# Kernel tuning notes

Measured on AMD Instinct MI355X. Metric: run time of the kernel, lower is better.

The kernel has to match this reference:

```python
import jax, jax.numpy as jnp
import numpy as np

N_NODES = 50000
N_EDGES = 1600000
SLOPE = 0.01  # LeakyReLU default negative slope


def _leaky(x):
    return jnp.where(x >= 0, x, SLOPE * x)


def _gcn(x, W, b, row, col, num_nodes):
    """PyG GCNConv: x' = D^{-1/2}(A+I)D^{-1/2} X W + b (self-loops already in row/col)."""
    x = x @ W  # [N, 64]
    deg = jax.ops.segment_sum(jnp.ones_like(row, dtype=x.dtype), col, num_segments=num_nodes)
    dinv = jnp.where(deg > 0, jax.lax.rsqrt(deg), 0.0)
    norm = dinv[row] * dinv[col]  # [E+N]
    msg = x[row] * norm[:, None]  # gather + scale, [E+N, 64]
    out = jax.ops.segment_sum(msg, col, num_segments=num_nodes)
    return out + b


def setup_inputs() -> dict:
    key = jax.random.key(0)
    ks = jax.random.split(key, 24)
    d = {}
    d["screen"] = jax.random.normal(ks[0], (N_NODES, 768), jnp.float32)
    d["des"] = jax.random.normal(ks[1], (N_NODES, 768), jnp.float32)
    d["tweet"] = jax.random.normal(ks[2], (N_NODES, 768), jnp.float32)
    d["profile"] = jax.random.normal(ks[3], (N_NODES, 5), jnp.float32)
    d["personal"] = jax.random.normal(ks[4], (N_NODES, 7), jnp.float32)
    d["edge"] = jax.random.randint(ks[5], (2, N_EDGES), 0, N_NODES, dtype=jnp.int32)

    def lin(k, fan_in, fan_out):
        s = 1.0 / np.sqrt(fan_in)
        k1, k2 = jax.random.split(k)
        W = jax.random.uniform(k1, (fan_in, fan_out), jnp.float32, -s, s)
        b = jax.random.uniform(k2, (fan_out,), jnp.float32, -s, s)
        return W, b

    d["W_screen"], d["b_screen"] = lin(ks[6], 768, 16)
    d["W_des"], d["b_des"] = lin(ks[7], 768, 16)
    d["W_tweet"], d["b_tweet"] = lin(ks[8], 768, 16)
    d["W_pro"], d["b_pro"] = lin(ks[9], 5, 8)
    d["W_per"], d["b_per"] = lin(ks[10], 7, 8)
    d["W_lin"], d["b_lin"] = lin(ks[11], 64, 64)
    d["W_g1"], d["b_g1"] = lin(ks[12], 64, 64)
    d["W_g2"], d["b_g2"] = lin(ks[13], 64, 64)
    d["W_g3"], d["b_g3"] = lin(ks[14], 64, 64)
    d["W_o1"], d["b_o1"] = lin(ks[15], 64, 64)
    d["W_o2"], d["b_o2"] = lin(ks[16], 64, 2)
    return d


def reference(screen, des, tweet, profile, personal, edge,
              W_screen, b_screen, W_des, b_des, W_tweet, b_tweet,
              W_pro, b_pro, W_per, b_per, W_lin, b_lin,
              W_g1, b_g1, W_g2, b_g2, W_g3, b_g3,
              W_o1, b_o1, W_o2, b_o2):
    n = screen.shape[0]
    # dropout layers act as identity in eval mode
    s = _leaky(screen @ W_screen + b_screen)
    de = _leaky(des @ W_des + b_des)
    t = _leaky(tweet @ W_tweet + b_tweet)
    p = _leaky(profile @ W_pro + b_pro)
    pe = _leaky(personal @ W_per + b_per)
    x1 = jnp.concatenate((s, de, t, p, pe), axis=1)  # [N, 64]
    x = _leaky(x1 @ W_lin + b_lin)
    # add self-loops once (shared by all three GCN layers)
    loops = jnp.arange(n, dtype=edge.dtype)
    row = jnp.concatenate([edge[0], loops])
    col = jnp.concatenate([edge[1], loops])
    x = _gcn(x, W_g1, b_g1, row, col, n) + x1
    x = _gcn(x, W_g2, b_g2, row, col, n) + x1
    x = _gcn(x, W_g3, b_g3, row, col, n) + x1
    x = _leaky(x @ W_o1 + b_o1)
    return jax.nn.sigmoid(x @ W_o2 + b_o2)
```

## Files before the change

### kernel.cpp

```cpp
#include <hip/hip_runtime.h>

__device__ __forceinline__ float leaky(float v) { return v >= 0.f ? v : 0.01f * v; }

__device__ __forceinline__ void fma4(float4& a, float s, const float4& w) {
    a.x = fmaf(s, w.x, a.x); a.y = fmaf(s, w.y, a.y);
    a.z = fmaf(s, w.z, a.z); a.w = fmaf(s, w.w, a.w);
}

__device__ __forceinline__ unsigned short f2bf(float x) {
    unsigned b = __float_as_uint(x);
    return (unsigned short)((b + 0x7FFFu + ((b >> 16) & 1u)) >> 16);
}
__device__ __forceinline__ float bf2f(unsigned short u) {
    return __uint_as_float(((unsigned)u) << 16);
}

typedef __attribute__((ext_vector_type(8))) short short8v;
typedef __attribute__((ext_vector_type(4))) float float4v;

__global__ void k_deg(const int* __restrict__ col, int E, int* __restrict__ deg) {
    int e = blockIdx.x * blockDim.x + threadIdx.x;
    if (e < E) atomicAdd(&deg[col[e]], 1);
}

__global__ __launch_bounds__(256) void k_scan_part(const int* __restrict__ deg,
                                                   int* __restrict__ part,
                                                   int* __restrict__ bsum, int N) {
    __shared__ int tmp[256];
    int tid = threadIdx.x;
    int i = blockIdx.x * 256 + tid;
    int v = (i < N) ? deg[i] : 0;
    tmp[tid] = v;
    __syncthreads();
    for (int ofs = 1; ofs < 256; ofs <<= 1) {
        int t = (tid >= ofs) ? tmp[tid - ofs] : 0;
        __syncthreads();
        tmp[tid] += t;
        __syncthreads();
    }
    int incl = tmp[tid];
    if (i < N) part[i] = incl - v;
    if (tid == 255) bsum[blockIdx.x] = incl;
}

__global__ __launch_bounds__(256) void k_scan_sums(const int* __restrict__ bsum,
                                                   int* __restrict__ boff, int NB,
                                                   int* __restrict__ offs_last) {
    __shared__ int tmp[256];
    int tid = threadIdx.x;
    int v = (tid < NB) ? bsum[tid] : 0;
    tmp[tid] = v;
    __syncthreads();
    for (int ofs = 1; ofs < 256; ofs <<= 1) {
        int t = (tid >= ofs) ? tmp[tid - ofs] : 0;
        __syncthreads();
        tmp[tid] += t;
        __syncthreads();
    }
    int incl = tmp[tid];
    if (tid < NB) boff[tid] = incl - v;
    if (tid == 255) offs_last[0] = incl;
}

__global__ __launch_bounds__(256) void k_scan_final(const int* __restrict__ part,
                                                    const int* __restrict__ boff,
                                                    const int* __restrict__ deg,
                                                    int* __restrict__ offs,
                                                    int* __restrict__ pos,
                                                    float* __restrict__ dinv, int N) {
    int i = blockIdx.x * 256 + threadIdx.x;
    if (i < N) {
        int o = part[i] + boff[blockIdx.x];
        offs[i] = o;
        pos[i] = o;
        dinv[i] = rsqrtf((float)(deg[i] + 1));
    }
}

__global__ void k_fill(const int* __restrict__ row, const int* __restrict__ col, int E,
                       int* __restrict__ pos, int* __restrict__ csr) {
    int e = blockIdx.x * blockDim.x + threadIdx.x;
    if (e < E) {
        int p = atomicAdd(&pos[col[e]], 1);
        csr[p] = row[e];
    }
}

__global__ __launch_bounds__(512) void k_featB(
    const float* __restrict__ s, const float* __restrict__ d, const float* __restrict__ t,
    const float* __restrict__ Ws, const float* __restrict__ bs2,
    const float* __restrict__ Wd, const float* __restrict__ bd2,
    const float* __restrict__ Wt, const float* __restrict__ bt2,
    const float* __restrict__ prof, const float* __restrict__ pers,
    const float* __restrict__ Wp, const float* __restrict__ bp,
    const float* __restrict__ Wpe, const float* __restrict__ bpe,
    float* __restrict__ x1g, int N, int NG) {
    __shared__ short8v wfv[3072];

    const int bid = blockIdx.x;
    const int tid = threadIdx.x;

    if (bid >= 3 * NG) {
        int n = (bid - 3 * NG) * 512 + tid;
        if (n >= N) return;
        float pv[5], pe[7];
#pragma unroll
        for (int i = 0; i < 5; ++i) pv[i] = prof[(size_t)n * 5 + i];
#pragma unroll
        for (int i = 0; i < 7; ++i) pe[i] = pers[(size_t)n * 7 + i];
        float o[16];
#pragma unroll
        for (int j = 0; j < 8; ++j) {
            float a = bp[j];
#pragma unroll
            for (int i = 0; i < 5; ++i) a = fmaf(pv[i], Wp[i * 8 + j], a);
            o[j] = leaky(a);
            float a2 = bpe[j];
#pragma unroll
            for (int i = 0; i < 7; ++i) a2 = fmaf(pe[i], Wpe[i * 8 + j], a2);
            o[8 + j] = leaky(a2);
        }
#pragma unroll
        for (int v = 0; v < 4; ++v)
            *reinterpret_cast<float4*>(x1g + (size_t)n * 64 + 48 + v * 4) =
                make_float4(o[v * 4], o[v * 4 + 1], o[v * 4 + 2], o[v * 4 + 3]);
        return;
    }

    const int f = bid / NG;
    const int grp = bid - f * NG;
    const float* __restrict__ X = (f == 0) ? s : ((f == 1) ? d : t);
    const float* __restrict__ W = (f == 0) ? Ws : ((f == 1) ? Wd : Wt);
    const float* __restrict__ B = (f == 0) ? bs2 : ((f == 1) ? bd2 : bt2);
    const int n0 = grp * 128;
    const int lane = tid & 63;
    const int wid = tid >> 6;

    short* wfs = (short*)wfv;
#pragma unroll
    for (int v = 0; v < 6; ++v) {
        int idx4 = tid + v * 512;
        float4 w4 = *reinterpret_cast<const float4*>(W + (size_t)idx4 * 4);
        int k = idx4 >> 2;
        int j0 = (idx4 & 3) * 4;
        int c = k >> 5, g = (k >> 3) & 3, i = k & 7;
        float wq[4] = {w4.x, w4.y, w4.z, w4.w};
#pragma unroll
        for (int q = 0; q < 4; ++q) {
            int sl = (c * 64 + g * 16 + j0 + q) * 8 + i;
            unsigned short h = f2bf(wq[q]);
            wfs[sl] = (short)h;
            wfs[12288 + sl] = (short)f2bf(wq[q] - bf2f(h));
        }
    }
    __syncthreads();

    const int nb = n0 + wid * 16;
    int mrow = nb + (lane & 15); if (mrow >= N) mrow = N - 1;
    const float* base = X + (size_t)mrow * 768 + ((lane >> 4) << 3);

    float4 pa[4], pb[4];
#pragma unroll
    for (int u = 0; u < 4; ++u) {
        pa[u] = *reinterpret_cast<const float4*>(base + u * 32);
        pb[u] = *reinterpret_cast<const float4*>(base + u * 32 + 4);
    }
    float4v acc = {0.f, 0.f, 0.f, 0.f};

#pragma unroll
    for (int c = 0; c < 24; ++c) {
        const int u = c & 3;
        float xs[8] = {pa[u].x, pa[u].y, pa[u].z, pa[u].w,
                       pb[u].x, pb[u].y, pb[u].z, pb[u].w};
        if (c + 4 < 24) {
            pa[u] = *reinterpret_cast<const float4*>(base + (c + 4) * 32);
            pb[u] = *reinterpret_cast<const float4*>(base + (c + 4) * 32 + 4);
        }
        short8v xh, xl;
#pragma unroll
        for (int i = 0; i < 8; ++i) {
            unsigned short h = f2bf(xs[i]);
            xh[i] = (short)h;
            xl[i] = (short)f2bf(xs[i] - bf2f(h));
        }
        short8v wh = wfv[c * 64 + lane];
        short8v wl = wfv[1536 + c * 64 + lane];
        acc = __builtin_amdgcn_mfma_f32_16x16x32_bf16(xh, wh, acc, 0, 0, 0);
        acc = __builtin_amdgcn_mfma_f32_16x16x32_bf16(xl, wh, acc, 0, 0, 0);
        acc = __builtin_amdgcn_mfma_f32_16x16x32_bf16(xh, wl, acc, 0, 0, 0);
    }

    int j = lane & 15;
    float bb = B[j];
#pragma unroll
    for (int r = 0; r < 4; ++r) {
        int n = nb + ((lane >> 4) << 2) + r;
        if (n < N) x1g[(size_t)n * 64 + f * 16 + j] = leaky(acc[r] + bb);
    }
}

__global__ __launch_bounds__(256) void k_lin1(const float* __restrict__ x1,
                                              const float* __restrict__ Wl,
                                              const float* __restrict__ bl,
                                              const float* __restrict__ Wg1,
                                              const float* __restrict__ dinvv,
                                              unsigned short* __restrict__ z, int N) {
    __shared__ float4 xt4[1024];
    __shared__ float4 wt4[1024];
    const int tid = threadIdx.x;
    const int n0 = blockIdx.x * 64;
    const int nq = tid & 15;
    const int jq = tid >> 4;

#pragma unroll
    for (int v = 0; v < 4; ++v) {
        int L = v * 256 + tid;
        int n = L >> 4, c4 = L & 15;
        int nn = n0 + n; if (nn >= N) nn = N - 1;
        xt4[n * 16 + (c4 ^ (n & 15))] = *reinterpret_cast<const float4*>(x1 + (size_t)nn * 64 + c4 * 4);
        wt4[L] = *reinterpret_cast<const float4*>(Wl + (size_t)L * 4);
    }
    __syncthreads();

    float4 acc[4];
#pragma unroll
    for (int g = 0; g < 4; ++g) acc[g] = make_float4(0.f, 0.f, 0.f, 0.f);
    for (int k = 0; k < 64; k += 4) {
        float4 w0 = wt4[(k + 0) * 16 + jq];
        float4 w1 = wt4[(k + 1) * 16 + jq];
        float4 w2 = wt4[(k + 2) * 16 + jq];
        float4 w3 = wt4[(k + 3) * 16 + jq];
        int k4 = k >> 2;
#pragma unroll
        for (int g = 0; g < 4; ++g) {
            int n = nq + (g << 4);
            float4 xv = xt4[n * 16 + (k4 ^ (n & 15))];
            fma4(acc[g], xv.x, w0);
            fma4(acc[g], xv.y, w1);
            fma4(acc[g], xv.z, w2);
            fma4(acc[g], xv.w, w3);
        }
    }
    float4 bb = *reinterpret_cast<const float4*>(bl + jq * 4);
    __syncthreads();

#pragma unroll
    for (int g = 0; g < 4; ++g) {
        int n = nq + (g << 4);
        float4 h;
        h.x = leaky(acc[g].x + bb.x);
        h.y = leaky(acc[g].y + bb.y);
        h.z = leaky(acc[g].z + bb.z);
        h.w = leaky(acc[g].w + bb.w);
        xt4[n * 16 + (jq ^ (n & 15))] = h;
    }
#pragma unroll
    for (int v = 0; v < 4; ++v) {
        int L = v * 256 + tid;
        wt4[L] = *reinterpret_cast<const float4*>(Wg1 + (size_t)L * 4);
    }
    __syncthreads();

#pragma unroll
    for (int g = 0; g < 4; ++g) acc[g] = make_float4(0.f, 0.f, 0.f, 0.f);
    for (int k = 0; k < 64; k += 4) {
        float4 w0 = wt4[(k + 0) * 16 + jq];
        float4 w1 = wt4[(k + 1) * 16 + jq];
        float4 w2 = wt4[(k + 2) * 16 + jq];
        float4 w3 = wt4[(k + 3) * 16 + jq];
        int k4 = k >> 2;
#pragma unroll
        for (int g = 0; g < 4; ++g) {
            int n = nq + (g << 4);
            float4 xv = xt4[n * 16 + (k4 ^ (n & 15))];
            fma4(acc[g], xv.x, w0);
            fma4(acc[g], xv.y, w1);
            fma4(acc[g], xv.z, w2);
            fma4(acc[g], xv.w, w3);
        }
    }
#pragma unroll
    for (int g = 0; g < 4; ++g) {
        int n = nq + (g << 4);
        if (n0 + n >= N) continue;
        float dv = dinvv[n0 + n];
        ushort4 o;
        o.x = f2bf(acc[g].x * dv); o.y = f2bf(acc[g].y * dv);
        o.z = f2bf(acc[g].z * dv); o.w = f2bf(acc[g].w * dv);
        *reinterpret_cast<ushort4*>(z + (size_t)(n0 + n) * 64 + jq * 4) = o;
    }
}

__global__ __launch_bounds__(256, 4) void k_mm64(const float* __restrict__ xin,
                                                 const float* __restrict__ W,
                                                 const float* __restrict__ dinvv,
                                                 unsigned short* __restrict__ z, int N) {
    __shared__ float4 xt4[1024];
    __shared__ float4 wt4[1024];
    const int tid = threadIdx.x;
    const int n0 = blockIdx.x * 64;
#pragma unroll
    for (int v = 0; v < 4; ++v) {
        int L = v * 256 + tid;
        int n = L >> 4, c4 = L & 15;
        int nn = n0 + n; if (nn >= N) nn = N - 1;
        xt4[n * 16 + (c4 ^ (n & 15))] = *reinterpret_cast<const float4*>(xin + (size_t)nn * 64 + c4 * 4);
        wt4[L] = *reinterpret_cast<const float4*>(W + (size_t)L * 4);
    }
    __syncthreads();
    const int nq = tid & 15;
    const int jq = tid >> 4;
    float4 acc[4];
#pragma unroll
    for (int g = 0; g < 4; ++g) acc[g] = make_float4(0.f, 0.f, 0.f, 0.f);
    for (int k = 0; k < 64; k += 4) {
        float4 w0 = wt4[(k + 0) * 16 + jq];
        float4 w1 = wt4[(k + 1) * 16 + jq];
        float4 w2 = wt4[(k + 2) * 16 + jq];
        float4 w3 = wt4[(k + 3) * 16 + jq];
        int k4 = k >> 2;
#pragma unroll
        for (int g = 0; g < 4; ++g) {
            int n = nq + (g << 4);
            float4 xv = xt4[n * 16 + (k4 ^ (n & 15))];
            fma4(acc[g], xv.x, w0);
            fma4(acc[g], xv.y, w1);
            fma4(acc[g], xv.z, w2);
            fma4(acc[g], xv.w, w3);
        }
    }
#pragma unroll
    for (int g = 0; g < 4; ++g) {
        int n = nq + (g << 4);
        if (n0 + n >= N) continue;
        float dv = dinvv[n0 + n];
        ushort4 o;
        o.x = f2bf(acc[g].x * dv); o.y = f2bf(acc[g].y * dv);
        o.z = f2bf(acc[g].z * dv); o.w = f2bf(acc[g].w * dv);
        *reinterpret_cast<ushort4*>(z + (size_t)(n0 + n) * 64 + jq * 4) = o;
    }
}

__global__ __launch_bounds__(256) void k_agg(const unsigned short* __restrict__ z,
                                             const int* __restrict__ offs,
                                             const int* __restrict__ csr,
                                             const float* __restrict__ dinv,
                                             const float* __restrict__ bias,
                                             const float* __restrict__ x1,
                                             float* __restrict__ xout, int N) {
    int lane = threadIdx.x & 63;
    int c = blockIdx.x * 4 + (threadIdx.x >> 6);
    if (c >= N) return;
    int s = __builtin_amdgcn_readfirstlane(offs[c]);
    int e = __builtin_amdgcn_readfirstlane(offs[c + 1]);
    const int half = lane >> 5;
    const int d = lane & 31;
    const unsigned* __restrict__ zr = (const unsigned*)z;

    float ax = 0.f, ay = 0.f;
    if (half == 0) {
        unsigned sv = zr[(size_t)c * 32 + d];
        ax = bf2f((unsigned short)(sv & 0xffffu));
        ay = bf2f((unsigned short)(sv >> 16));
    }
    float ux[8] = {0, 0, 0, 0, 0, 0, 0, 0};
    float uy[8] = {0, 0, 0, 0, 0, 0, 0, 0};
    int j = s;
    for (; j + 16 <= e; j += 16) {
#pragma unroll
        for (int u = 0; u < 8; ++u) {
            int r0 = csr[j + 2 * u];
            int r1 = csr[j + 2 * u + 1];
            int r = half ? r1 : r0;
            unsigned v = zr[(size_t)r * 32 + d];
            ux[u] += bf2f((unsigned short)(v & 0xffffu));
            uy[u] += bf2f((unsigned short)(v >> 16));
        }
    }
    for (; j + 2 <= e; j += 2) {
        int r0 = csr[j];
        int r1 = csr[j + 1];
        int r = half ? r1 : r0;
        unsigned v = zr[(size_t)r * 32 + d];
        ax += bf2f((unsigned short)(v & 0xffffu));
        ay += bf2f((unsigned short)(v >> 16));
    }
    if (j < e && half == 0) {
        int r = csr[j];
        unsigned v = zr[(size_t)r * 32 + d];
        ax += bf2f((unsigned short)(v & 0xffffu));
        ay += bf2f((unsigned short)(v >> 16));
    }
    float tx = ax + ((ux[0] + ux[1]) + (ux[2] + ux[3])) + ((ux[4] + ux[5]) + (ux[6] + ux[7]));
    float ty = ay + ((uy[0] + uy[1]) + (uy[2] + uy[3])) + ((uy[4] + uy[5]) + (uy[6] + uy[7]));
    tx += __shfl_xor(tx, 32);
    ty += __shfl_xor(ty, 32);
    if (half == 0) {
        float dv = dinv[c];
        float2 bb = reinterpret_cast<const float2*>(bias)[d];
        float2 xx = *reinterpret_cast<const float2*>(x1 + (size_t)c * 64 + 2 * d);
        float2 o;
        o.x = dv * tx + bb.x + xx.x;
        o.y = dv * ty + bb.y + xx.y;
        *reinterpret_cast<float2*>(xout + (size_t)c * 64 + 2 * d) = o;
    }
}

__global__ __launch_bounds__(256) void k_head(const float* __restrict__ xin,
                                              const float* __restrict__ Wo1,
                                              const float* __restrict__ bo1,
                                              const float* __restrict__ Wo2,
                                              const float* __restrict__ bo2,
                                              float* __restrict__ out, int N) {
    __shared__ float xsg[64][65];
    __shared__ float wg[64][65];
    __shared__ float hs[64][65];
    __shared__ float wo2[128];
    const int tid = threadIdx.x;
    const int n0 = blockIdx.x * 64;
#pragma unroll
    for (int v = 0; v < 4; ++v) {
        int idx = tid + v * 256;
        int n = idx >> 4;
        int jj = (idx & 15) << 2;
        float4 xv = make_float4(0.f, 0.f, 0.f, 0.f);
        if (n0 + n < N) xv = *reinterpret_cast<const float4*>(xin + (size_t)(n0 + n) * 64 + jj);
        xsg[n][jj] = xv.x; xsg[n][jj + 1] = xv.y; xsg[n][jj + 2] = xv.z; xsg[n][jj + 3] = xv.w;
        float4 w = *reinterpret_cast<const float4*>(Wo1 + (size_t)n * 64 + jj);
        wg[n][jj] = w.x; wg[n][jj + 1] = w.y; wg[n][jj + 2] = w.z; wg[n][jj + 3] = w.w;
    }
    if (tid < 128) wo2[tid] = Wo2[tid];
    __syncthreads();
    int j = tid & 63;
    int g = tid >> 6;
    float bj = bo1[j];
    for (int i = 0; i < 16; ++i) {
        int n = g * 16 + i;
        float a = bj;
#pragma unroll
        for (int k = 0; k < 64; ++k) a += xsg[n][k] * wg[k][j];
        hs[n][j] = leaky(a);
    }
    __syncthreads();
    if (tid < 128) {
        int n = tid >> 1;
        int j2 = tid & 1;
        float a = bo2[j2];
#pragma unroll
        for (int k = 0; k < 64; ++k) a += hs[n][k] * wo2[k * 2 + j2];
        if (n0 + n < N) out[(size_t)(n0 + n) * 2 + j2] = 1.f / (1.f + expf(-a));
    }
}

extern "C" void kernel_launch(void* const* d_in, const int* in_sizes, int n_in,
                              void* d_out, int out_size, void* d_ws, size_t ws_size,
                              hipStream_t stream) {
    const float* screen   = (const float*)d_in[0];
    const float* des      = (const float*)d_in[1];
    const float* tweet    = (const float*)d_in[2];
    const float* profile  = (const float*)d_in[3];
    const float* personal = (const float*)d_in[4];
    const int*   edge     = (const int*)d_in[5];
    const float* Ws  = (const float*)d_in[6],  *bs  = (const float*)d_in[7];
    const float* Wd  = (const float*)d_in[8],  *bd  = (const float*)d_in[9];
    const float* Wt  = (const float*)d_in[10], *bt  = (const float*)d_in[11];
    const float* Wp  = (const float*)d_in[12], *bp  = (const float*)d_in[13];
    const float* Wpe = (const float*)d_in[14], *bpe = (const float*)d_in[15];
    const float* Wl  = (const float*)d_in[16], *bl  = (const float*)d_in[17];
    const float* Wg1 = (const float*)d_in[18], *bg1 = (const float*)d_in[19];
    const float* Wg2 = (const float*)d_in[20], *bg2 = (const float*)d_in[21];
    const float* Wg3 = (const float*)d_in[22], *bg3 = (const float*)d_in[23];
    const float* Wo1 = (const float*)d_in[24], *bo1 = (const float*)d_in[25];
    const float* Wo2 = (const float*)d_in[26], *bo2 = (const float*)d_in[27];

    const int N = in_sizes[0] / 768;
    const int E = in_sizes[5] / 2;
    const int* row = edge;
    const int* col = edge + E;

    size_t off = 0;
    auto alloc = [&](size_t bytes) -> void* {
        void* p = (char*)d_ws + off;
        off += (bytes + 255) & ~(size_t)255;
        return p;
    };
    const size_t NF = (size_t)N * 64;
    float* x1   = (float*)alloc(NF * 4);
    float* xa   = (float*)alloc(NF * 4);
    float* xb   = (float*)alloc(NF * 4);
    unsigned short* z = (unsigned short*)alloc(NF * 2);
    float* dinv = (float*)alloc((size_t)N * 4);
    int* deg  = (int*)alloc((size_t)N * 4);
    int* part = (int*)alloc((size_t)N * 4);
    int* offs = (int*)alloc((size_t)(N + 1) * 4);
    int* pos  = (int*)alloc((size_t)N * 4);
    int* csr  = (int*)alloc((size_t)E * 4);
    const int NB = (N + 255) / 256;
    int* bsum = (int*)alloc((size_t)NB * 4);
    int* boff = (int*)alloc((size_t)NB * 4);
    (void)ws_size; (void)n_in; (void)out_size;

    hipMemsetAsync(deg, 0, (size_t)N * 4, stream);
    k_deg<<<(E + 255) / 256, 256, 0, stream>>>(col, E, deg);
    k_scan_part<<<NB, 256, 0, stream>>>(deg, part, bsum, N);
    k_scan_sums<<<1, 256, 0, stream>>>(bsum, boff, NB, offs + N);
    k_scan_final<<<NB, 256, 0, stream>>>(part, boff, deg, offs, pos, dinv, N);
    k_fill<<<(E + 255) / 256, 256, 0, stream>>>(row, col, E, pos, csr);

    const int NG = (N + 127) / 128;
    const int NSM = (N + 511) / 512;
    k_featB<<<NG * 3 + NSM, 512, 0, stream>>>(screen, des, tweet,
                                              Ws, bs, Wd, bd, Wt, bt,
                                              profile, personal, Wp, bp, Wpe, bpe,
                                              x1, N, NG);

    const int NGB = (N + 63) / 64;
    const int NAB = (N + 3) / 4;
    k_lin1<<<NGB, 256, 0, stream>>>(x1, Wl, bl, Wg1, dinv, z, N);
    k_agg<<<NAB, 256, 0, stream>>>(z, offs, csr, dinv, bg1, x1, xb, N);
    k_mm64<<<NGB, 256, 0, stream>>>(xb, Wg2, dinv, z, N);
    k_agg<<<NAB, 256, 0, stream>>>(z, offs, csr, dinv, bg2, x1, xa, N);
    k_mm64<<<NGB, 256, 0, stream>>>(xa, Wg3, dinv, z, N);
    k_agg<<<NAB, 256, 0, stream>>>(z, offs, csr, dinv, bg3, x1, xb, N);

    k_head<<<NGB, 256, 0, stream>>>(xb, Wo1, bo1, Wo2, bo2, (float*)d_out, N);
}
```

Before: 478.9 us.

## Aggregate four neighbors per wave with 8-byte loads; add waves_per_eu hint to featB

The CSR aggregation kernel now splits each 64-lane wave into four 16-lane groups. Each lane loads a ushort4 (four bf16 features), so a wave gathers four neighbor rows at once instead of two. The partial sums are combined with two xor shuffles and written as float4. This is meant to give wider loads and more memory-level parallelism per wave for the roughly 32 neighbors per node, at the cost of more accumulator registers. Separately, the feature kernel gets an amdgpu_waves_per_eu(4,6) occupancy hint.

```diff
diff --git a/kernel.cpp b/kernel.cpp
--- a/kernel.cpp
+++ b/kernel.cpp
@@ -86,7 +86,8 @@
     }
 }
 
-__global__ __launch_bounds__(512) void k_featB(
+__global__ __attribute__((amdgpu_waves_per_eu(4, 6))) __launch_bounds__(512)
+void k_featB(
     const float* __restrict__ s, const float* __restrict__ d, const float* __restrict__ t,
     const float* __restrict__ Ws, const float* __restrict__ bs2,
     const float* __restrict__ Wd, const float* __restrict__ bd2,
@@ -353,56 +354,57 @@
     if (c >= N) return;
     int s = __builtin_amdgcn_readfirstlane(offs[c]);
     int e = __builtin_amdgcn_readfirstlane(offs[c + 1]);
-    const int half = lane >> 5;
-    const int d = lane & 31;
-    const unsigned* __restrict__ zr = (const unsigned*)z;
-
-    float ax = 0.f, ay = 0.f;
-    if (half == 0) {
-        unsigned sv = zr[(size_t)c * 32 + d];
-        ax = bf2f((unsigned short)(sv & 0xffffu));
-        ay = bf2f((unsigned short)(sv >> 16));
-    }
-    float ux[8] = {0, 0, 0, 0, 0, 0, 0, 0};
-    float uy[8] = {0, 0, 0, 0, 0, 0, 0, 0};
+    const int q = lane >> 4;
+    const int d = lane & 15;
+    const ushort4* __restrict__ zr = (const ushort4*)z;
+
+    float4 a = make_float4(0.f, 0.f, 0.f, 0.f);
+    if (q == 0) {
+        ushort4 v = zr[(size_t)c * 16 + d];
+        a.x = bf2f(v.x); a.y = bf2f(v.y); a.z = bf2f(v.z); a.w = bf2f(v.w);
+    }
+    float4 u[8];
+#pragma unroll
+    for (int t = 0; t < 8; ++t) u[t] = make_float4(0.f, 0.f, 0.f, 0.f);
+
     int j = s;
-    for (; j + 16 <= e; j += 16) {
-#pragma unroll
-        for (int u = 0; u < 8; ++u) {
-            int r0 = csr[j + 2 * u];
-            int r1 = csr[j + 2 * u + 1];
-            int r = half ? r1 : r0;
-            unsigned v = zr[(size_t)r * 32 + d];
-            ux[u] += bf2f((unsigned short)(v & 0xffffu));
-            uy[u] += bf2f((unsigned short)(v >> 16));
-        }
-    }
-    for (; j + 2 <= e; j += 2) {
-        int r0 = csr[j];
-        int r1 = csr[j + 1];
-        int r = half ? r1 : r0;
-        unsigned v = zr[(size_t)r * 32 + d];
-        ax += bf2f((unsigned short)(v & 0xffffu));
-        ay += bf2f((unsigned short)(v >> 16));
-    }
-    if (j < e && half == 0) {
-        int r = csr[j];
-        unsigned v = zr[(size_t)r * 32 + d];
-        ax += bf2f((unsigned short)(v & 0xffffu));
-        ay += bf2f((unsigned short)(v >> 16));
-    }
-    float tx = ax + ((ux[0] + ux[1]) + (ux[2] + ux[3])) + ((ux[4] + ux[5]) + (ux[6] + ux[7]));
-    float ty = ay + ((uy[0] + uy[1]) + (uy[2] + uy[3])) + ((uy[4] + uy[5]) + (uy[6] + uy[7]));
-    tx += __shfl_xor(tx, 32);
-    ty += __shfl_xor(ty, 32);
-    if (half == 0) {
+    for (; j + 32 <= e; j += 32) {
+#pragma unroll
+        for (int t = 0; t < 8; ++t) {
+            int r = csr[j + 4 * t + q];
+            ushort4 v = zr[(size_t)r * 16 + d];
+            u[t].x += bf2f(v.x); u[t].y += bf2f(v.y);
+            u[t].z += bf2f(v.z); u[t].w += bf2f(v.w);
+        }
+    }
+    for (; j + 4 <= e; j += 4) {
+        int r = csr[j + q];
+        ushort4 v = zr[(size_t)r * 16 + d];
+        a.x += bf2f(v.x); a.y += bf2f(v.y); a.z += bf2f(v.z); a.w += bf2f(v.w);
+    }
+    if (j < e && q < e - j) {
+        int r = csr[j + q];
+        ushort4 v = zr[(size_t)r * 16 + d];
+        a.x += bf2f(v.x); a.y += bf2f(v.y); a.z += bf2f(v.z); a.w += bf2f(v.w);
+    }
+    float tx = a.x + ((u[0].x + u[1].x) + (u[2].x + u[3].x)) + ((u[4].x + u[5].x) + (u[6].x + u[7].x));
+    float ty = a.y + ((u[0].y + u[1].y) + (u[2].y + u[3].y)) + ((u[4].y + u[5].y) + (u[6].y + u[7].y));
+    float tz = a.z + ((u[0].z + u[1].z) + (u[2].z + u[3].z)) + ((u[4].z + u[5].z) + (u[6].z + u[7].z));
+    float tw = a.w + ((u[0].w + u[1].w) + (u[2].w + u[3].w)) + ((u[4].w + u[5].w) + (u[6].w + u[7].w));
+    tx += __shfl_xor(tx, 16); tx += __shfl_xor(tx, 32);
+    ty += __shfl_xor(ty, 16); ty += __shfl_xor(ty, 32);
+    tz += __shfl_xor(tz, 16); tz += __shfl_xor(tz, 32);
+    tw += __shfl_xor(tw, 16); tw += __shfl_xor(tw, 32);
+    if (q == 0) {
         float dv = dinv[c];
-        float2 bb = reinterpret_cast<const float2*>(bias)[d];
-        float2 xx = *reinterpret_cast<const float2*>(x1 + (size_t)c * 64 + 2 * d);
-        float2 o;
+        float4 bb = reinterpret_cast<const float4*>(bias)[d];
+        float4 xx = *reinterpret_cast<const float4*>(x1 + (size_t)c * 64 + 4 * d);
+        float4 o;
         o.x = dv * tx + bb.x + xx.x;
         o.y = dv * ty + bb.y + xx.y;
-        *reinterpret_cast<float2*>(xout + (size_t)c * 64 + 2 * d) = o;
+        o.z = dv * tz + bb.z + xx.z;
+        o.w = dv * tw + bb.w + xx.w;
+        *reinterpret_cast<float4*>(xout + (size_t)c * 64 + 4 * d) = o;
     }
 }
 
```

New measurement: 530.4 us. +10.8%, slower.

## Fold degree counting and CSR fill into feature and lin1 kernels

Applied to the files above, without the earlier changes.

Removes the standalone degree-count and CSR-fill kernels. Their work now runs as extra blocks appended to the k_featB and k_lin1 grids, so the atomic-bound graph construction overlaps with the compute-heavy feature projection and first linear layer, and two launches disappear. The risk is that the atomic blocks compete with the GEMM blocks for CUs and memory bandwidth. The appended blocks also inherit the host kernels' launch shape (512 threads and large shared memory for featB), which can lower occupancy for those simple blocks.

```diff
diff --git a/kernel.cpp b/kernel.cpp
--- a/kernel.cpp
+++ b/kernel.cpp
@@ -17,11 +17,6 @@
 
 typedef __attribute__((ext_vector_type(8))) short short8v;
 typedef __attribute__((ext_vector_type(4))) float float4v;
-
-__global__ void k_deg(const int* __restrict__ col, int E, int* __restrict__ deg) {
-    int e = blockIdx.x * blockDim.x + threadIdx.x;
-    if (e < E) atomicAdd(&deg[col[e]], 1);
-}
 
 __global__ __launch_bounds__(256) void k_scan_part(const int* __restrict__ deg,
                                                    int* __restrict__ part,
@@ -77,15 +72,6 @@
     }
 }
 
-__global__ void k_fill(const int* __restrict__ row, const int* __restrict__ col, int E,
-                       int* __restrict__ pos, int* __restrict__ csr) {
-    int e = blockIdx.x * blockDim.x + threadIdx.x;
-    if (e < E) {
-        int p = atomicAdd(&pos[col[e]], 1);
-        csr[p] = row[e];
-    }
-}
-
 __global__ __launch_bounds__(512) void k_featB(
     const float* __restrict__ s, const float* __restrict__ d, const float* __restrict__ t,
     const float* __restrict__ Ws, const float* __restrict__ bs2,
@@ -94,11 +80,18 @@
     const float* __restrict__ prof, const float* __restrict__ pers,
     const float* __restrict__ Wp, const float* __restrict__ bp,
     const float* __restrict__ Wpe, const float* __restrict__ bpe,
-    float* __restrict__ x1g, int N, int NG) {
+    const int* __restrict__ colv, int* __restrict__ deg, int E,
+    float* __restrict__ x1g, int N, int NG, int NSM) {
     __shared__ short8v wfv[3072];
 
     const int bid = blockIdx.x;
     const int tid = threadIdx.x;
+
+    if (bid >= 3 * NG + NSM) {
+        int e = (bid - 3 * NG - NSM) * 512 + tid;
+        if (e < E) atomicAdd(&deg[colv[e]], 1);
+        return;
+    }
 
     if (bid >= 3 * NG) {
         int n = (bid - 3 * NG) * 512 + tid;
@@ -204,11 +197,27 @@
                                               const float* __restrict__ bl,
                                               const float* __restrict__ Wg1,
                                               const float* __restrict__ dinvv,
-                                              unsigned short* __restrict__ z, int N) {
+                                              const int* __restrict__ rowv,
+                                              const int* __restrict__ colv,
+                                              int* __restrict__ pos,
+                                              int* __restrict__ csr, int E,
+                                              unsigned short* __restrict__ z,
+                                              int N, int NGB) {
     __shared__ float4 xt4[1024];
     __shared__ float4 wt4[1024];
     const int tid = threadIdx.x;
-    const int n0 = blockIdx.x * 64;
+    const int bid = blockIdx.x;
+
+    if (bid >= NGB) {
+        int e = (bid - NGB) * 256 + tid;
+        if (e < E) {
+            int p = atomicAdd(&pos[colv[e]], 1);
+            csr[p] = rowv[e];
+        }
+        return;
+    }
+
+    const int n0 = bid * 64;
     const int nq = tid & 15;
     const int jq = tid >> 4;
 
@@ -501,22 +510,25 @@
     (void)ws_size; (void)n_in; (void)out_size;
 
     hipMemsetAsync(deg, 0, (size_t)N * 4, stream);
-    k_deg<<<(E + 255) / 256, 256, 0, stream>>>(col, E, deg);
+
+    const int NG = (N + 127) / 128;
+    const int NSM = (N + 511) / 512;
+    const int NDEG = (E + 511) / 512;
+    k_featB<<<NG * 3 + NSM + NDEG, 512, 0, stream>>>(screen, des, tweet,
+                                                     Ws, bs, Wd, bd, Wt, bt,
+                                                     profile, personal, Wp, bp, Wpe, bpe,
+                                                     col, deg, E,
+                                                     x1, N, NG, NSM);
+
     k_scan_part<<<NB, 256, 0, stream>>>(deg, part, bsum, N);
     k_scan_sums<<<1, 256, 0, stream>>>(bsum, boff, NB, offs + N);
     k_scan_final<<<NB, 256, 0, stream>>>(part, boff, deg, offs, pos, dinv, N);
-    k_fill<<<(E + 255) / 256, 256, 0, stream>>>(row, col, E, pos, csr);
-
-    const int NG = (N + 127) / 128;
-    const int NSM = (N + 511) / 512;
-    k_featB<<<NG * 3 + NSM, 512, 0, stream>>>(screen, des, tweet,
-                                              Ws, bs, Wd, bd, Wt, bt,
-                                              profile, personal, Wp, bp, Wpe, bpe,
-                                              x1, N, NG);
 
     const int NGB = (N + 63) / 64;
+    const int NFILL = (E + 255) / 256;
     const int NAB = (N + 3) / 4;
-    k_lin1<<<NGB, 256, 0, stream>>>(x1, Wl, bl, Wg1, dinv, z, N);
+    k_lin1<<<NGB + NFILL, 256, 0, stream>>>(x1, Wl, bl, Wg1, dinv,
+                                            row, col, pos, csr, E, z, N, NGB);
     k_agg<<<NAB, 256, 0, stream>>>(z, offs, csr, dinv, bg1, x1, xb, N);
     k_mm64<<<NGB, 256, 0, stream>>>(xb, Wg2, dinv, z, N);
     k_agg<<<NAB, 256, 0, stream>>>(z, offs, csr, dinv, bg2, x1, xa, N);
```

After: 475.3 us. About the same (-0.8%).
